# Kernel tuning notes

Measured on AMD Instinct MI355X. Metric: run time of the kernel, lower is better.

The kernel has to match this reference:

```python
import jax, jax.numpy as jnp
import numpy as np
import math

D_MODEL = 1024
NUM_HEAD = 16
D_HEAD = D_MODEL // NUM_HEAD
SEQ = 2048
BATCH = 2


def setup_inputs() -> dict:
    key = jax.random.key(0)
    k1, k2, k3, k4, k5 = jax.random.split(key, 5)
    s = 1.0 / math.sqrt(D_MODEL)
    return {
        "x": jax.random.normal(k1, (SEQ, BATCH, D_MODEL), dtype=jnp.float32),
        "qkv_w": jax.random.normal(k2, (3 * D_MODEL, D_MODEL), dtype=jnp.float32) * s,
        "qkv_b": jax.random.normal(k3, (3 * D_MODEL,), dtype=jnp.float32) * 0.01,
        "out_w": jax.random.normal(k4, (D_MODEL, D_MODEL), dtype=jnp.float32) * s,
        "out_b": jax.random.normal(k5, (D_MODEL,), dtype=jnp.float32) * 0.01,
        "is_causal": 1,
    }


def reference(x, qkv_w, qkv_b, out_w, out_b, is_causal):
    t, b, _ = x.shape
    qkv = x @ qkv_w.T + qkv_b  # [t, b, 3*d_model]
    # 't b (k h d) -> b k h t d'
    qkv = qkv.reshape(t, b, 3, NUM_HEAD, D_HEAD).transpose(1, 2, 3, 0, 4)
    q, k, v = qkv[:, 0], qkv[:, 1], qkv[:, 2]  # each [b, h, t, d]
    softmax_scale = 1.0 / math.sqrt(D_HEAD)
    # NOTE: faithful to source bug: score is DIVIDED by softmax_scale
    score = jnp.einsum('bhtd,bhsd->bhts', q, k) / softmax_scale
    if is_causal:
        causal_mask = jnp.triu(jnp.full((t, t), -1000000.0, dtype=score.dtype), k=1)
        score = score + causal_mask
    attn = jax.nn.softmax(score, axis=-1)
    av = jnp.einsum('bhts,bhsd->bhtd', attn, v)  # [b, h, t, d]
    av = av.transpose(2, 0, 1, 3).reshape(t, b, D_MODEL)  # 'b h t d -> t b (h d)'
    return av @ out_w.T + out_b
```

## Files before the change

kernel.cpp:

```cpp
#include <hip/hip_runtime.h>
#include <math.h>

#define TSEQ   2048
#define BB     2
#define DMODEL 1024
#define NHEAD  16
#define DHEAD  64
#define MROWS  (TSEQ * BB)

typedef __attribute__((ext_vector_type(8))) _Float16 half8;
typedef __attribute__((ext_vector_type(4))) float    floatx4;
typedef unsigned short u16;
typedef unsigned int   u32;

#define QSCL 11.5415603f
#define MSK  1442695.0f

__device__ __forceinline__ u16 f2h(float f) {
    union { _Float16 h; u16 u; } cv;
    cv.h = (_Float16)f;
    return cv.u;
}

__device__ __forceinline__ u32 pkrtz(float a, float b) {
    typedef __attribute__((ext_vector_type(2))) __fp16 fp16x2;
    union { fp16x2 h; u32 u; } cv;
    cv.h = __builtin_amdgcn_cvt_pkrtz(a, b);
    return cv.u;
}

__device__ __forceinline__ void async_cp16(const u16* g, u16* l) {
    __builtin_amdgcn_global_load_lds(
        (const __attribute__((address_space(1))) unsigned int*)g,
        (__attribute__((address_space(3))) unsigned int*)l, 16, 0, 0);
}

__global__ __launch_bounds__(256)
void cast3_f32_f16(const float* __restrict__ a, u16* __restrict__ oa,
                   const float* __restrict__ b, u16* __restrict__ ob,
                   const float* __restrict__ c, u16* __restrict__ oc)
{
    int i = blockIdx.x * 256 + threadIdx.x;
    const float* src; u16* dst; int off;
    if (i < 1048576)      { src = a; dst = oa; off = 0; }
    else if (i < 1835008) { src = b; dst = ob; off = 1048576; }
    else                  { src = c; dst = oc; off = 1835008; }
    int j = i - off;
    float4 v = ((const float4*)src)[j];
    ushort4 o;
    o.x = f2h(v.x); o.y = f2h(v.y); o.z = f2h(v.z); o.w = f2h(v.w);
    ((ushort4*)dst)[j] = o;
}

__global__ __launch_bounds__(256)
void gemm_qkv(const u16* __restrict__ A, const u16* __restrict__ W,
              const float* __restrict__ bias,
              u16* __restrict__ Qo, u16* __restrict__ Ko, u16* __restrict__ Vo,
              int M, int N, int K)
{
    __shared__ __align__(16) u16 As[128][64];
    __shared__ __align__(16) u16 Bs[64][64];

    const int tid  = threadIdx.x;
    const int lane = tid & 63;
    const int wv   = tid >> 6;
    const int ln   = lane & 15, lh = lane >> 4;

    const int bidlin = blockIdx.y * 48 + blockIdx.x;
    const int wg  = (bidlin & 7) * 192 + (bidlin >> 3);
    const int bx  = wg % 48, by = wg / 48;
    const int m0  = by * 128;
    const int n0  = bx * 64;

    const int c = n0 >> 10;
    const bool vmode = (c == 2);

    const int srowA = wv * 32 + (lane >> 3);
    const int srowW = wv * 16 + (lane >> 3);
    const int sslot = lane & 7;

    const floatx4 zero4 = {0.0f, 0.0f, 0.0f, 0.0f};
    floatx4 acc[2][4];
#pragma unroll
    for (int i = 0; i < 2; ++i)
#pragma unroll
        for (int j = 0; j < 4; ++j) acc[i][j] = zero4;

    for (int k0 = 0; k0 < K; k0 += 64) {
        __syncthreads();
#pragma unroll
        for (int t = 0; t < 4; ++t) {
            const int row = srowA + t * 8;
            const int g   = sslot ^ (row & 7);
            async_cp16(A + (size_t)(m0 + row) * K + k0 + g * 8, &As[row][sslot * 8]);
        }
#pragma unroll
        for (int t = 0; t < 2; ++t) {
            const int row = srowW + t * 8;
            const int g   = sslot ^ (row & 7);
            async_cp16(W + (size_t)(n0 + row) * K + k0 + g * 8, &Bs[row][sslot * 8]);
        }
        __syncthreads();

#pragma unroll
        for (int ks = 0; ks < 2; ++ks) {
            half8 xf[2], wf[4];
#pragma unroll
            for (int i = 0; i < 2; ++i) {
                const int row = wv * 32 + i * 16 + ln;
                xf[i] = *(const half8*)&As[row][(((ks << 2) | lh) ^ (row & 7)) * 8];
            }
#pragma unroll
            for (int j = 0; j < 4; ++j) {
                const int row = j * 16 + ln;
                wf[j] = *(const half8*)&Bs[row][(((ks << 2) | lh) ^ (row & 7)) * 8];
            }
            if (vmode) {
#pragma unroll
                for (int i = 0; i < 2; ++i)
#pragma unroll
                    for (int j = 0; j < 4; ++j)
                        acc[i][j] = __builtin_amdgcn_mfma_f32_16x16x32_f16(xf[i], wf[j], acc[i][j], 0, 0, 0);
            } else {
#pragma unroll
                for (int i = 0; i < 2; ++i)
#pragma unroll
                    for (int j = 0; j < 4; ++j)
                        acc[i][j] = __builtin_amdgcn_mfma_f32_16x16x32_f16(wf[j], xf[i], acc[i][j], 0, 0, 0);
            }
        }
    }

    if (!vmode) {
        const float scl = (c == 0) ? QSCL : 1.0f;
        u16* dst = (c == 0) ? Qo : Ko;
#pragma unroll
        for (int j = 0; j < 4; ++j) {
            const int nb = n0 + j * 16 + lh * 4;
            const float4 b4 = *(const float4*)&bias[nb];
            const int h  = (nb >> 6) & 15;
            const int d0 = nb & 63;
#pragma unroll
            for (int i = 0; i < 2; ++i) {
                const int tok = m0 + wv * 32 + i * 16 + ln;
                const int t = tok >> 1, b = tok & 1;
                uint2 pk;
                pk.x = pkrtz((acc[i][j][0] + b4.x) * scl, (acc[i][j][1] + b4.y) * scl);
                pk.y = pkrtz((acc[i][j][2] + b4.z) * scl, (acc[i][j][3] + b4.w) * scl);
                *(uint2*)&dst[(((size_t)b * NHEAD + h) * TSEQ + t) * DHEAD + d0] = pk;
            }
        }
    } else {
#pragma unroll
        for (int j = 0; j < 4; ++j) {
            const int col = n0 + j * 16 + ln;
            const float bc = bias[col];
            const int h = (col >> 6) & 15;
            const int d = col & 63;
#pragma unroll
            for (int i = 0; i < 2; ++i) {
                const int mb = m0 + wv * 32 + i * 16 + lh * 4;
                const int t0 = mb >> 1;
                const u32 e0 = pkrtz(acc[i][j][0] + bc, acc[i][j][2] + bc);
                const u32 e1 = pkrtz(acc[i][j][1] + bc, acc[i][j][3] + bc);
                *(u32*)&Vo[(((size_t)0 * NHEAD + h) * DHEAD + d) * TSEQ + t0] = e0;
                *(u32*)&Vo[(((size_t)1 * NHEAD + h) * DHEAD + d) * TSEQ + t0] = e1;
            }
        }
    }
}

__global__ __launch_bounds__(256)
void gemm_out64(const u16* __restrict__ A, const u16* __restrict__ W,
                const float* __restrict__ bias, float* __restrict__ Cout,
                int M, int N, int K)
{
    __shared__ __align__(16) u16 As[64][64];
    __shared__ __align__(16) u16 Bs[64][64];

    const int tid  = threadIdx.x;
    const int lane = tid & 63;
    const int wv   = tid >> 6;
    const int ln   = lane & 15, lh = lane >> 4;

    const int bidlin = blockIdx.y * 16 + blockIdx.x;
    const int wg  = (bidlin & 7) * 128 + (bidlin >> 3);
    const int bx  = wg & 15, by = wg >> 4;
    const int m0  = by * 64;
    const int n0  = bx * 64;

    const floatx4 zero4 = {0.0f, 0.0f, 0.0f, 0.0f};
    floatx4 acc[4];
#pragma unroll
    for (int j = 0; j < 4; ++j) acc[j] = zero4;

    for (int k0 = 0; k0 < K; k0 += 64) {
        __syncthreads();
#pragma unroll
        for (int cb = 0; cb < 2; ++cb) {
            const int idx  = cb * 256 + tid;
            const int row  = idx >> 3;
            const int slot = idx & 7;
            const int g    = slot ^ (row & 7);
            async_cp16(A + (size_t)(m0 + row) * K + k0 + g * 8, &As[row][slot * 8]);
            async_cp16(W + (size_t)(n0 + row) * K + k0 + g * 8, &Bs[row][slot * 8]);
        }
        __syncthreads();

#pragma unroll
        for (int ks = 0; ks < 2; ++ks) {
            const int arow = wv * 16 + ln;
            half8 xf = *(const half8*)&As[arow][(((ks << 2) | lh) ^ (arow & 7)) * 8];
#pragma unroll
            for (int j = 0; j < 4; ++j) {
                const int row = j * 16 + ln;
                half8 wf = *(const half8*)&Bs[row][(((ks << 2) | lh) ^ (row & 7)) * 8];
                acc[j] = __builtin_amdgcn_mfma_f32_16x16x32_f16(wf, xf, acc[j], 0, 0, 0);
            }
        }
    }

#pragma unroll
    for (int j = 0; j < 4; ++j) {
        const int fb = n0 + j * 16 + lh * 4;
        const float4 b4 = *(const float4*)&bias[fb];
        const int tok = m0 + wv * 16 + ln;
        float4 v;
        v.x = acc[j][0] + b4.x;
        v.y = acc[j][1] + b4.y;
        v.z = acc[j][2] + b4.z;
        v.w = acc[j][3] + b4.w;
        *(float4*)&Cout[(size_t)tok * N + fb] = v;
    }
}

__global__ __launch_bounds__(256, 4)
void flash_f16(const u16* __restrict__ Q, const u16* __restrict__ K,
               const u16* __restrict__ Vt, u16* __restrict__ AV,
               const int* __restrict__ causal_p)
{
    __shared__ __align__(16) u16 smem[192 * 72];
    u16 (* __restrict__ Ps)[72] = (u16(*)[72])smem;
    u16 (* __restrict__ Ks)[72] = (u16(*)[72])(smem + 64 * 72);
    u16 (* __restrict__ Vs)[72] = (u16(*)[72])(smem + 128 * 72);

    const int tid  = threadIdx.x;
    const int lane = tid & 63;
    const int wv   = tid >> 6;
    const int ln   = lane & 15, lh = lane >> 4;

    const int phase = blockIdx.x >> 8;
    const int slot  = blockIdx.x & 255;
    const int bh    = slot & 31;
    const int jq    = slot >> 5;
    int qb;
    if      (phase == 0) qb = 31 - jq;
    else if (phase == 1) qb = jq;
    else if (phase == 2) qb = 23 - jq;
    else                 qb = 8 + jq;

    const int b = bh >> 4;
    const int h = bh & 15;
    const int causal = causal_p[0];

    const u16* Qg = Q  + (size_t)bh * TSEQ * DHEAD;
    const u16* Kg = K  + (size_t)bh * TSEQ * DHEAD;
    const u16* Vg = Vt + (size_t)bh * DHEAD * TSEQ;

    const int lrow = tid >> 3;
    const int lc8  = (tid & 7) * 8;

    const int qr0   = wv * 16;
    const int qloc  = qr0 + ln;
    const int qglob = qb * 64 + qloc;

    const half8 bQ0 = *(const half8*)(Qg + (size_t)qglob * DHEAD + lh * 8);
    const half8 bQ1 = *(const half8*)(Qg + (size_t)qglob * DHEAD + 32 + lh * 8);

    const _Float16 ov = (_Float16)((ln == 0) ? 1.0f : 0.0f);
    const half8 ones = {ov, ov, ov, ov, ov, ov, ov, ov};

    const floatx4 zero4 = {0.0f, 0.0f, 0.0f, 0.0f};
    floatx4 o[4], o4;
#pragma unroll
    for (int j = 0; j < 4; ++j) o[j] = zero4;
    o4 = zero4;
    float m_i = -3.0e38f;

    const int kb_end = causal ? qb : (TSEQ / 64 - 1);

    uint4 kreg0 = *(const uint4*)(Kg + (size_t)lrow * DHEAD + lc8);
    uint4 kreg1 = *(const uint4*)(Kg + (size_t)(lrow + 32) * DHEAD + lc8);
    uint4 vreg0 = *(const uint4*)(Vg + (size_t)lrow * TSEQ + lc8);
    uint4 vreg1 = *(const uint4*)(Vg + (size_t)(lrow + 32) * TSEQ + lc8);

    for (int kb = 0; kb <= kb_end; ++kb) {
        *(uint4*)&Ks[lrow][lc8]      = kreg0;
        *(uint4*)&Ks[lrow + 32][lc8] = kreg1;
        *(uint4*)&Vs[lrow][lc8]      = vreg0;
        *(uint4*)&Vs[lrow + 32][lc8] = vreg1;
        __syncthreads();

        if (kb < kb_end) {
            const size_t nk = (size_t)(kb + 1) * 64;
            kreg0 = *(const uint4*)(Kg + (nk + lrow) * DHEAD + lc8);
            kreg1 = *(const uint4*)(Kg + (nk + lrow + 32) * DHEAD + lc8);
            vreg0 = *(const uint4*)(Vg + (size_t)lrow * TSEQ + nk + lc8);
            vreg1 = *(const uint4*)(Vg + (size_t)(lrow + 32) * TSEQ + nk + lc8);
        }

        floatx4 s[4];
        __builtin_amdgcn_s_setprio(1);
#pragma unroll
        for (int j = 0; j < 4; ++j) {
            half8 aK0 = *(const half8*)&Ks[j * 16 + ln][lh * 8];
            half8 aK1 = *(const half8*)&Ks[j * 16 + ln][32 + lh * 8];
            floatx4 z = zero4;
            z = __builtin_amdgcn_mfma_f32_16x16x32_f16(aK0, bQ0, z, 0, 0, 0);
            z = __builtin_amdgcn_mfma_f32_16x16x32_f16(aK1, bQ1, z, 0, 0, 0);
            s[j] = z;
        }
        __builtin_amdgcn_s_setprio(0);

        half8 bV[8];
#pragma unroll
        for (int j = 0; j < 4; ++j) {
            bV[2 * j]     = *(const half8*)&Vs[j * 16 + ln][lh * 8];
            bV[2 * j + 1] = *(const half8*)&Vs[j * 16 + ln][32 + lh * 8];
        }

        if ((causal != 0) && (kb == qb)) {
#pragma unroll
            for (int j = 0; j < 4; ++j)
#pragma unroll
                for (int r = 0; r < 4; ++r)
                    if (j * 16 + lh * 4 + r > qloc) s[j][r] -= MSK;
        }

        float mx = m_i;
#pragma unroll
        for (int j = 0; j < 4; ++j)
#pragma unroll
            for (int r = 0; r < 4; ++r) mx = fmaxf(mx, s[j][r]);
        mx = fmaxf(mx, __shfl_xor(mx, 16));
        mx = fmaxf(mx, __shfl_xor(mx, 32));

        if (!__all(mx <= m_i + 8.0f)) {
            const float alpha = exp2f(m_i - mx);
            m_i = mx;
            float a_r[4];
#pragma unroll
            for (int r = 0; r < 4; ++r) a_r[r] = __shfl(alpha, lh * 4 + r);
#pragma unroll
            for (int j = 0; j < 4; ++j)
#pragma unroll
                for (int r = 0; r < 4; ++r) o[j][r] *= a_r[r];
#pragma unroll
            for (int r = 0; r < 4; ++r) o4[r] *= a_r[r];
        }

#pragma unroll
        for (int j = 0; j < 4; ++j) {
            uint2 pk;
            pk.x = pkrtz(exp2f(s[j][0] - m_i), exp2f(s[j][1] - m_i));
            pk.y = pkrtz(exp2f(s[j][2] - m_i), exp2f(s[j][3] - m_i));
            *(uint2*)&Ps[qloc][j * 16 + lh * 4] = pk;
        }

        half8 aP0 = *(const half8*)&Ps[qloc][lh * 8];
        half8 aP1 = *(const half8*)&Ps[qloc][32 + lh * 8];
        __builtin_amdgcn_s_setprio(1);
#pragma unroll
        for (int j = 0; j < 4; ++j) {
            o[j] = __builtin_amdgcn_mfma_f32_16x16x32_f16(aP0, bV[2 * j],     o[j], 0, 0, 0);
            o[j] = __builtin_amdgcn_mfma_f32_16x16x32_f16(aP1, bV[2 * j + 1], o[j], 0, 0, 0);
        }
        o4 = __builtin_amdgcn_mfma_f32_16x16x32_f16(aP0, ones, o4, 0, 0, 0);
        o4 = __builtin_amdgcn_mfma_f32_16x16x32_f16(aP1, ones, o4, 0, 0, 0);
        __builtin_amdgcn_s_setprio(0);

        __syncthreads();
    }

#pragma unroll
    for (int r = 0; r < 4; ++r) {
        const float lr = __shfl(o4[r], lane & 48);
        const float il = 1.0f / lr;
        const int qrow = qb * 64 + qr0 + lh * 4 + r;
#pragma unroll
        for (int j = 0; j < 4; ++j) {
            const int d = j * 16 + ln;
            AV[((size_t)qrow * BB + b) * DMODEL + h * 64 + d] = f2h(o[j][r] * il);
        }
    }
}

extern "C" void kernel_launch(void* const* d_in, const int* in_sizes, int n_in,
                              void* d_out, int out_size, void* d_ws, size_t ws_size,
                              hipStream_t stream)
{
    const float* x      = (const float*)d_in[0];
    const float* qkv_w  = (const float*)d_in[1];
    const float* qkv_b  = (const float*)d_in[2];
    const float* out_w  = (const float*)d_in[3];
    const float* out_b  = (const float*)d_in[4];
    const int*   is_causal = (const int*)d_in[5];
    float* out = (float*)d_out;

    u16* ws   = (u16*)d_ws;
    u16* xb   = ws;
    u16* wqkv = xb   + (size_t)4194304;
    u16* wout = wqkv + (size_t)3145728;
    u16* Qh   = wout + (size_t)1048576;
    u16* Kh   = Qh   + (size_t)4194304;
    u16* Vth  = Kh   + (size_t)4194304;
    u16* AVh  = Vth  + (size_t)4194304;

    cast3_f32_f16<<<8192, 256, 0, stream>>>(x, xb, qkv_w, wqkv, out_w, wout);

    gemm_qkv<<<dim3(3 * DMODEL / 64, MROWS / 128), 256, 0, stream>>>(
        xb, wqkv, qkv_b, Qh, Kh, Vth, MROWS, 3 * DMODEL, DMODEL);

    flash_f16<<<1024, 256, 0, stream>>>(Qh, Kh, Vth, AVh, is_causal);

    gemm_out64<<<dim3(DMODEL / 64, MROWS / 64), 256, 0, stream>>>(
        AVh, wout, out_b, out, MROWS, DMODEL, DMODEL);
}
```

Baseline: 185.6 us.

## Split-K output projection with atomic accumulation and drop QKV block swizzle

The output projection GEMM is split into two K halves along a new grid z dimension, each accumulating into the output with float atomics. A separate fill_bias kernel first initializes the output with the bias. The QKV GEMM block-index swizzle is removed in favour of direct blockIdx mapping. This is meant to double the block count of the small output GEMM for better occupancy. In exchange it adds an extra kernel launch, a full write pass over the output, atomic traffic and nondeterministic summation order.

```diff
diff --git a/kernel.cpp b/kernel.cpp
--- a/kernel.cpp
+++ b/kernel.cpp
@@ -53,6 +53,13 @@
 }
 
 __global__ __launch_bounds__(256)
+void fill_bias(const float* __restrict__ bias, float* __restrict__ out)
+{
+    const int j = blockIdx.x * 256 + threadIdx.x;
+    ((float4*)out)[j] = ((const float4*)bias)[j & 255];
+}
+
+__global__ __launch_bounds__(256)
 void gemm_qkv(const u16* __restrict__ A, const u16* __restrict__ W,
               const float* __restrict__ bias,
               u16* __restrict__ Qo, u16* __restrict__ Ko, u16* __restrict__ Vo,
@@ -65,12 +72,8 @@
     const int lane = tid & 63;
     const int wv   = tid >> 6;
     const int ln   = lane & 15, lh = lane >> 4;
-
-    const int bidlin = blockIdx.y * 48 + blockIdx.x;
-    const int wg  = (bidlin & 7) * 192 + (bidlin >> 3);
-    const int bx  = wg % 48, by = wg / 48;
-    const int m0  = by * 128;
-    const int n0  = bx * 64;
+    const int m0   = blockIdx.y * 128;
+    const int n0   = blockIdx.x * 64;
 
     const int c = n0 >> 10;
     const bool vmode = (c == 2);
@@ -172,8 +175,7 @@
 
 __global__ __launch_bounds__(256)
 void gemm_out64(const u16* __restrict__ A, const u16* __restrict__ W,
-                const float* __restrict__ bias, float* __restrict__ Cout,
-                int M, int N, int K)
+                float* __restrict__ Cout, int M, int N, int K)
 {
     __shared__ __align__(16) u16 As[64][64];
     __shared__ __align__(16) u16 Bs[64][64];
@@ -188,13 +190,15 @@
     const int bx  = wg & 15, by = wg >> 4;
     const int m0  = by * 64;
     const int n0  = bx * 64;
+    const int kz  = blockIdx.z;
 
     const floatx4 zero4 = {0.0f, 0.0f, 0.0f, 0.0f};
     floatx4 acc[4];
 #pragma unroll
     for (int j = 0; j < 4; ++j) acc[j] = zero4;
 
-    for (int k0 = 0; k0 < K; k0 += 64) {
+    const int kbeg = kz * 512;
+    for (int k0 = kbeg; k0 < kbeg + 512; k0 += 64) {
         __syncthreads();
 #pragma unroll
         for (int cb = 0; cb < 2; ++cb) {
@@ -222,15 +226,13 @@
 
 #pragma unroll
     for (int j = 0; j < 4; ++j) {
-        const int fb = n0 + j * 16 + lh * 4;
-        const float4 b4 = *(const float4*)&bias[fb];
+        const int fb  = n0 + j * 16 + lh * 4;
         const int tok = m0 + wv * 16 + ln;
-        float4 v;
-        v.x = acc[j][0] + b4.x;
-        v.y = acc[j][1] + b4.y;
-        v.z = acc[j][2] + b4.z;
-        v.w = acc[j][3] + b4.w;
-        *(float4*)&Cout[(size_t)tok * N + fb] = v;
+        float* dst = &Cout[(size_t)tok * N + fb];
+        atomicAdd(dst + 0, acc[j][0]);
+        atomicAdd(dst + 1, acc[j][1]);
+        atomicAdd(dst + 2, acc[j][2]);
+        atomicAdd(dst + 3, acc[j][3]);
     }
 }
 
@@ -423,6 +425,7 @@
 
     flash_f16<<<1024, 256, 0, stream>>>(Qh, Kh, Vth, AVh, is_causal);
 
-    gemm_out64<<<dim3(DMODEL / 64, MROWS / 64), 256, 0, stream>>>(
-        AVh, wout, out_b, out, MROWS, DMODEL, DMODEL);
-}
+    fill_bias<<<4096, 256, 0, stream>>>(out_b, out);
+    gemm_out64<<<dim3(DMODEL / 64, MROWS / 64, 2), 256, 0, stream>>>(
+        AVh, wout, out, MROWS, DMODEL, DMODEL);
+}
```

Result: slower. 294.3 us (+58.6%).
